# Kernel optimization log

Measured on AMD Instinct MI355X. Metric: run time of the kernel, lower is better.

Reference implementation:

```python
import jax, jax.numpy as jnp
import numpy as np

N_TYPES = 4
N_PAIRS = N_TYPES * N_TYPES          # 16 (src_type, dst_type) pairs
N_GLOBAL_ET = 24                     # global edge event types
N_LOCAL_ET = 16                      # per-pair predictor output classes
D = 256                              # hidden dim
E = 262144                           # number of edges


def setup_inputs() -> dict:
    key = jax.random.key(0)
    ks = jax.random.split(key, 12)
    s = 0.05
    h_src = jax.random.normal(ks[0], (E, D), jnp.float32)
    h_dst = jax.random.normal(ks[1], (E, D), jnp.float32)
    src_type_idx = jax.random.randint(ks[2], (E,), 0, N_TYPES)
    dst_type_idx = jax.random.randint(ks[3], (E,), 0, N_TYPES)
    edge_type_classes = jax.random.randint(ks[4], (E,), 0, N_GLOBAL_ET)
    # decoder params: Linear(concat(h_src,h_dst)) -> D, split into two matrices
    W1 = jax.random.normal(ks[5], (D, D), jnp.float32) * s
    W2 = jax.random.normal(ks[6], (D, D), jnp.float32) * s
    b_dec = jnp.zeros((D,), jnp.float32)
    # per-(src,dst)-pair predictor heads, stacked
    W_pred = jax.random.normal(ks[7], (N_PAIRS, D, N_LOCAL_ET), jnp.float32) * s
    b_pred = jnp.zeros((N_PAIRS, N_LOCAL_ET), jnp.float32)
    # event_map[pair, global_edge_type] -> local class id
    event_map = jax.random.randint(ks[8], (N_PAIRS, N_GLOBAL_ET), 0, N_LOCAL_ET)
    return {
        'h_src': h_src, 'h_dst': h_dst,
        'W1': W1, 'W2': W2, 'b_dec': b_dec,
        'W_pred': W_pred, 'b_pred': b_pred,
        'src_type_idx': src_type_idx, 'dst_type_idx': dst_type_idx,
        'edge_type_classes': edge_type_classes, 'event_map': event_map,
        'inference': 0,
    }


def reference(h_src, h_dst, W1, W2, b_dec, W_pred, b_pred,
              src_type_idx, dst_type_idx, edge_type_classes, event_map,
              inference):
    # decoder: Linear(concat(h_src, h_dst)) -> D, ReLU
    h = jax.nn.relu(h_src @ W1 + h_dst @ W2 + b_dec)            # [E, D]
    pair = src_type_idx * N_TYPES + dst_type_idx                 # [E]
    # grouped per-pair linear heads: compute all heads, select per-edge head
    logits_all = jnp.einsum('ed,pdc->epc', h, W_pred) + b_pred   # [E, P, C]
    logits = jnp.take_along_axis(
        logits_all, pair[:, None, None], axis=1)[:, 0]           # [E, C]
    labels = event_map[pair, edge_type_classes]                  # [E]
    logp = jax.nn.log_softmax(logits, axis=-1)
    per_edge_loss = -jnp.take_along_axis(logp, labels[:, None], axis=1)[:, 0]
    # training path: per-group mean, then mean over non-empty groups
    sums = jax.ops.segment_sum(per_edge_loss, pair, num_segments=N_PAIRS)
    cnts = jax.ops.segment_sum(jnp.ones_like(per_edge_loss), pair,
                               num_segments=N_PAIRS)
    present = cnts > 0
    gmean = jnp.where(present, sums / jnp.maximum(cnts, 1.0), 0.0)
    loss = jnp.sum(gmean) / jnp.sum(present.astype(jnp.float32))
    return loss
```

## Files before the change

kernel.cpp:

```cpp
#include <hip/hip_runtime.h>
#include <stdint.h>

#define E_EDGES 262144
#define TILE_M 128
#define MAX_TILES 2064

typedef unsigned short ushort_t;
typedef __attribute__((ext_vector_type(8))) short short8;
typedef __attribute__((ext_vector_type(4))) float f32x4;

#define OFF_WT   0
#define OFF_WP   (512*256*2)
#define OFF_PERM (OFF_WP + 16*8*64*8*2)
#define OFF_HIST (OFF_PERM + MAX_TILES*128*4)
#define OFF_SEG  (OFF_HIST + 64)
#define OFF_CUR  (OFF_SEG + 128)
#define OFF_SUMS (OFF_CUR + 64)

__device__ __forceinline__ ushort_t f2bf(float f) {
  union { float f; unsigned u; } c; c.f = f;
  unsigned r = c.u + 0x7fffu + ((c.u >> 16) & 1u);
  return (ushort_t)(r >> 16);
}

__device__ __forceinline__ void async_copy16(void* lds, const void* g) {
  __builtin_amdgcn_global_load_lds(
      (const __attribute__((address_space(1))) unsigned int*)g,
      (__attribute__((address_space(3))) unsigned int*)lds, 16, 0, 0);
}

__global__ __launch_bounds__(256) void prep_k(const float* __restrict__ W1,
    const float* __restrict__ W2, const float* __restrict__ Wp,
    char* __restrict__ ws) {
  const int i = blockIdx.x * 256 + threadIdx.x;
  int* perm = (int*)(ws + OFF_PERM);
  if (i < MAX_TILES * 128) perm[i] = -1;
  if (i < 512 * 256) {
    ushort_t* Wt = (ushort_t*)(ws + OFF_WT);
    const int n = i >> 9, k = i & 511;
    const float v = (k < 256) ? W1[(k << 8) + n] : W2[((k - 256) << 8) + n];
    Wt[i] = f2bf(v);
  }
  if (i < 16 * 8 * 64 * 8) {
    ushort_t* Wpf = (ushort_t*)(ws + OFF_WP);
    const int j = i & 7, l = (i >> 3) & 63, s = (i >> 9) & 7, p = i >> 12;
    const int k = s * 32 + (l >> 4) * 8 + j, c = l & 15;
    Wpf[i] = f2bf(Wp[((p << 8) + k) * 16 + c]);
  }
  if (i < 16) {
    ((int*)(ws + OFF_HIST))[i] = 0;
    ((int*)(ws + OFF_CUR))[i] = 0;
    ((float*)(ws + OFF_SUMS))[i] = 0.f;
  }
}

__global__ __launch_bounds__(256) void hist_k(const int* __restrict__ st,
    const int* __restrict__ dt, char* __restrict__ ws) {
  __shared__ int lh[16];
  int* hist = (int*)(ws + OFF_HIST);
  const int t = threadIdx.x;
  if (t < 16) lh[t] = 0;
  __syncthreads();
  const int i = blockIdx.x * 256 + t;
  if (i < E_EDGES) atomicAdd(&lh[st[i] * 4 + dt[i]], 1);
  __syncthreads();
  if (t < 16 && lh[t] > 0) atomicAdd(&hist[t], lh[t]);
}

__global__ void scan_k(char* __restrict__ ws) {
  if (threadIdx.x == 0) {
    const int* hist = (const int*)(ws + OFF_HIST);
    int* seg = (int*)(ws + OFF_SEG);
    int acc = 0;
    for (int p = 0; p < 16; ++p) {
      seg[p] = acc;
      acc += (hist[p] + 127) & ~127;
    }
    seg[16] = acc;
  }
}

__global__ __launch_bounds__(256) void scatter_k(const int* __restrict__ st,
    const int* __restrict__ dt, char* __restrict__ ws) {
  __shared__ int lh[16], lbase[16];
  const int* seg = (const int*)(ws + OFF_SEG);
  int* cur = (int*)(ws + OFF_CUR);
  int* perm = (int*)(ws + OFF_PERM);
  const int t = threadIdx.x;
  if (t < 16) lh[t] = 0;
  __syncthreads();
  const int i = blockIdx.x * 256 + t;
  int p = 0, r = 0;
  const bool v = (i < E_EDGES);
  if (v) { p = st[i] * 4 + dt[i]; r = atomicAdd(&lh[p], 1); }
  __syncthreads();
  if (t < 16 && lh[t] > 0) lbase[t] = atomicAdd(&cur[t], lh[t]);
  __syncthreads();
  if (v) perm[seg[p] + lbase[p] + r] = i;
}

__global__ __launch_bounds__(512, 4) void main_k(
    const float* __restrict__ h_src, const float* __restrict__ h_dst,
    const float* __restrict__ b_dec, const float* __restrict__ b_pred,
    const int* __restrict__ etc_arr, const int* __restrict__ emap,
    char* __restrict__ ws) {
  const ushort_t* Wt = (const ushort_t*)(ws + OFF_WT);
  const short8* Wpf = (const short8*)(ws + OFF_WP);
  const int* perm = (const int*)(ws + OFF_PERM);
  const int* seg = (const int*)(ws + OFF_SEG);
  float* sums = (float*)(ws + OFF_SUMS);

  const int tb = blockIdx.x * TILE_M;
  if (tb >= seg[16]) return;
  int pair = 0;
#pragma unroll
  for (int p = 1; p < 16; ++p) pair += (tb >= seg[p]) ? 1 : 0;

  __shared__ __align__(16) char smem[65536];
  ushort_t* A_buf0 = (ushort_t*)smem;
  ushort_t* A_buf1 = (ushort_t*)(smem + 10240);
  char* B_buf0 = smem + 20480;
  char* B_buf1 = smem + 36864;
  ushort_t* H_ls = (ushort_t*)smem;

  const int t = threadIdx.x;
  const int w = t >> 6, lane = t & 63;
  const int quad = lane >> 4, l15 = lane & 15;
  const int wm = w >> 2, wn = w & 3;

  const int arow = t >> 2, acg = t & 3;
  const int e_stage = perm[tb + arow];
  const int e_safe = (e_stage < 0) ? 0 : e_stage;

  const f32x4 zero4 = {0.f, 0.f, 0.f, 0.f};
  f32x4 acc[4][4];
#pragma unroll
  for (int i = 0; i < 4; ++i)
#pragma unroll
    for (int j = 0; j < 4; ++j) acc[i][j] = zero4;

  auto stage_B = [&](int kt, char* Bb) {
#pragma unroll
    for (int ci = 0; ci < 2; ++ci) {
      const int chunk = w * 2 + ci;
      const int n = chunk * 16 + l15;
      const int k = kt * 32 + quad * 8;
      async_copy16(Bb + chunk * 1024, Wt + n * 512 + k);
    }
  };
  auto gather_A = [&](int kt, f32x4* fv) {
    const float* srcb = (kt < 8) ? h_src : h_dst;
    const f32x4* gp = (const f32x4*)(srcb + ((size_t)e_safe << 8) + (kt & 7) * 32 + acg * 8);
    fv[0] = gp[0];
    fv[1] = gp[1];
  };
  auto conv_write = [&](const f32x4* fv, ushort_t* Ab) {
    union { ushort_t u[8]; short8 v; } pk;
#pragma unroll
    for (int q = 0; q < 2; ++q)
#pragma unroll
      for (int x = 0; x < 4; ++x) pk.u[q * 4 + x] = f2bf(fv[q][x]);
    *(short8*)(Ab + arow * 40 + acg * 8) = pk.v;
  };
  auto mma_step = [&](const ushort_t* Ab, const char* Bb) {
    short8 a[4];
#pragma unroll
    for (int i = 0; i < 4; ++i)
      a[i] = *(const short8*)(Ab + (wm * 64 + i * 16 + l15) * 40 + quad * 8);
#pragma unroll
    for (int j = 0; j < 4; ++j) {
      const short8 b = *(const short8*)(Bb + (wn * 4 + j) * 1024 + lane * 16);
#pragma unroll
      for (int i = 0; i < 4; ++i)
        acc[i][j] = __builtin_amdgcn_mfma_f32_16x16x32_bf16(a[i], b, acc[i][j], 0, 0, 0);
    }
  };

  f32x4 ga0[2], ga1[2];
  gather_A(0, ga0);
  __builtin_amdgcn_sched_barrier(0);
  stage_B(0, B_buf0);
  __builtin_amdgcn_sched_barrier(0);
  gather_A(1, ga1);
  __builtin_amdgcn_sched_barrier(0);
  conv_write(ga0, A_buf0);
  asm volatile("s_waitcnt vmcnt(2) lgkmcnt(0)" ::: "memory");
  __builtin_amdgcn_s_barrier();
  __builtin_amdgcn_sched_barrier(0);

#pragma unroll
  for (int kt = 0; kt < 15; ++kt) {
    ushort_t* Acur = (kt & 1) ? A_buf1 : A_buf0;
    ushort_t* Anxt = (kt & 1) ? A_buf0 : A_buf1;
    char* Bcur = (kt & 1) ? B_buf1 : B_buf0;
    char* Bnxt = (kt & 1) ? B_buf0 : B_buf1;
    f32x4* g_nxt = (kt & 1) ? ga0 : ga1;
    f32x4* g_new = (kt & 1) ? ga1 : ga0;

    stage_B(kt + 1, Bnxt);
    __builtin_amdgcn_sched_barrier(0);
    gather_A(kt + 2, g_new);
    __builtin_amdgcn_sched_barrier(0);
    mma_step(Acur, Bcur);
    asm volatile("s_waitcnt vmcnt(4)" ::: "memory");
    conv_write(g_nxt, Anxt);
    asm volatile("s_waitcnt vmcnt(2) lgkmcnt(0)" ::: "memory");
    __builtin_amdgcn_s_barrier();
    __builtin_amdgcn_sched_barrier(0);
  }
  mma_step(A_buf1, B_buf1);
  __syncthreads();

  float bj[4];
#pragma unroll
  for (int j = 0; j < 4; ++j) bj[j] = b_dec[wn * 64 + j * 16 + l15];
#pragma unroll
  for (int i = 0; i < 4; ++i)
#pragma unroll
    for (int j = 0; j < 4; ++j)
#pragma unroll
      for (int r = 0; r < 4; ++r) {
        const int row = wm * 64 + i * 16 + quad * 4 + r;
        const int col = wn * 64 + j * 16 + l15;
        float v = acc[i][j][r] + bj[j];
        v = fmaxf(v, 0.f);
        H_ls[row * 256 + col] = f2bf(v);
      }
  __syncthreads();

  f32x4 acc2 = zero4;
#pragma unroll
  for (int s = 0; s < 8; ++s) {
    short8 a = *(const short8*)(H_ls + (w * 16 + l15) * 256 + s * 32 + quad * 8);
    short8 b = Wpf[(pair * 8 + s) * 64 + lane];
    acc2 = __builtin_amdgcn_mfma_f32_16x16x32_bf16(a, b, acc2, 0, 0, 0);
  }

  const float bp = b_pred[pair * 16 + l15];
  float wacc = 0.f;
#pragma unroll
  for (int r = 0; r < 4; ++r) {
    const int row = w * 16 + quad * 4 + r;
    const int e = perm[tb + row];
    float v = acc2[r] + bp;
    float m = v;
#pragma unroll
    for (int o = 1; o < 16; o <<= 1) m = fmaxf(m, __shfl_xor(m, o, 16));
    float sm = __expf(v - m);
#pragma unroll
    for (int o = 1; o < 16; o <<= 1) sm += __shfl_xor(sm, o, 16);
    int label = 0;
    if (e >= 0) label = emap[pair * 24 + etc_arr[e]];
    const float vlab = __shfl(v, (lane & 48) + label, 64);
    if (e >= 0 && l15 == 0) wacc += m + __logf(sm) - vlab;
  }
  wacc += __shfl_xor(wacc, 16, 64);
  wacc += __shfl_xor(wacc, 32, 64);
  if (lane == 0) atomicAdd(&sums[pair], wacc);
}

__global__ void finalize_k(const char* __restrict__ ws, float* __restrict__ out) {
  const float* sums = (const float*)(ws + OFF_SUMS);
  const int* hist = (const int*)(ws + OFF_HIST);
  const int t = threadIdx.x;
  float g = 0.f, pr = 0.f;
  if (t < 16) {
    const int c = hist[t];
    if (c > 0) { g = sums[t] / (float)c; pr = 1.f; }
  }
#pragma unroll
  for (int o = 1; o < 16; o <<= 1) { g += __shfl_xor(g, o, 64); pr += __shfl_xor(pr, o, 64); }
  if (t == 0) out[0] = g / pr;
}

extern "C" void kernel_launch(void* const* d_in, const int* in_sizes, int n_in,
                              void* d_out, int out_size, void* d_ws, size_t ws_size,
                              hipStream_t stream) {
  const float* h_src  = (const float*)d_in[0];
  const float* h_dst  = (const float*)d_in[1];
  const float* W1     = (const float*)d_in[2];
  const float* W2     = (const float*)d_in[3];
  const float* b_dec  = (const float*)d_in[4];
  const float* W_pred = (const float*)d_in[5];
  const float* b_pred = (const float*)d_in[6];
  const int* st   = (const int*)d_in[7];
  const int* dt   = (const int*)d_in[8];
  const int* etc  = (const int*)d_in[9];
  const int* emap = (const int*)d_in[10];
  char* ws = (char*)d_ws;
  float* out = (float*)d_out;

  prep_k<<<(MAX_TILES * 128 + 255) / 256, 256, 0, stream>>>(W1, W2, W_pred, ws);
  hist_k<<<E_EDGES / 256, 256, 0, stream>>>(st, dt, ws);
  scan_k<<<1, 64, 0, stream>>>(ws);
  scatter_k<<<E_EDGES / 256, 256, 0, stream>>>(st, dt, ws);
  main_k<<<MAX_TILES, 512, 0, stream>>>(h_src, h_dst, b_dec, b_pred, etc, emap, ws);
  finalize_k<<<1, 64, 0, stream>>>(ws, out);
}
```

Before: 740.8 us.

## Compute all pair heads per tile and drop the edge sorting pipeline

Removes the histogram, scan and scatter kernels that grouped edges by pair, and processes edges in their natural order. Each tile now computes logits for all 16 pair heads with a 128x256 MFMA GEMM and selects each edge's head per row, accumulating per-pair sums and counts in shared memory before global atomics. It also adds an XOR swizzle to the H tile in LDS to reduce bank conflicts. This trades extra MFMA work on the second GEMM for removing three kernel launches, the permutation indirection, padding tiles and scattered gathers.

Measured after the change: 612.3 us. 1.21x faster.

```diff
diff --git a/kernel.cpp b/kernel.cpp
--- a/kernel.cpp
+++ b/kernel.cpp
@@ -3,7 +3,7 @@
 
 #define E_EDGES 262144
 #define TILE_M 128
-#define MAX_TILES 2064
+#define NBLK (E_EDGES / TILE_M)
 
 typedef unsigned short ushort_t;
 typedef __attribute__((ext_vector_type(8))) short short8;
@@ -11,11 +11,8 @@
 
 #define OFF_WT   0
 #define OFF_WP   (512*256*2)
-#define OFF_PERM (OFF_WP + 16*8*64*8*2)
-#define OFF_HIST (OFF_PERM + MAX_TILES*128*4)
-#define OFF_SEG  (OFF_HIST + 64)
-#define OFF_CUR  (OFF_SEG + 128)
-#define OFF_SUMS (OFF_CUR + 64)
+#define OFF_HIST (OFF_WP + 8*16*64*8*2)
+#define OFF_SUMS (OFF_HIST + 64)
 
 __device__ __forceinline__ ushort_t f2bf(float f) {
   union { float f; unsigned u; } c; c.f = f;
@@ -33,90 +30,40 @@
     const float* __restrict__ W2, const float* __restrict__ Wp,
     char* __restrict__ ws) {
   const int i = blockIdx.x * 256 + threadIdx.x;
-  int* perm = (int*)(ws + OFF_PERM);
-  if (i < MAX_TILES * 128) perm[i] = -1;
   if (i < 512 * 256) {
     ushort_t* Wt = (ushort_t*)(ws + OFF_WT);
     const int n = i >> 9, k = i & 511;
     const float v = (k < 256) ? W1[(k << 8) + n] : W2[((k - 256) << 8) + n];
     Wt[i] = f2bf(v);
   }
-  if (i < 16 * 8 * 64 * 8) {
+  if (i < 8 * 16 * 64 * 8) {
     ushort_t* Wpf = (ushort_t*)(ws + OFF_WP);
-    const int j = i & 7, l = (i >> 3) & 63, s = (i >> 9) & 7, p = i >> 12;
-    const int k = s * 32 + (l >> 4) * 8 + j, c = l & 15;
+    const int jj = i & 7, l = (i >> 3) & 63, p = (i >> 9) & 15, s = i >> 13;
+    const int k = s * 32 + (l >> 4) * 8 + jj, c = l & 15;
     Wpf[i] = f2bf(Wp[((p << 8) + k) * 16 + c]);
   }
   if (i < 16) {
     ((int*)(ws + OFF_HIST))[i] = 0;
-    ((int*)(ws + OFF_CUR))[i] = 0;
     ((float*)(ws + OFF_SUMS))[i] = 0.f;
   }
-}
-
-__global__ __launch_bounds__(256) void hist_k(const int* __restrict__ st,
-    const int* __restrict__ dt, char* __restrict__ ws) {
-  __shared__ int lh[16];
-  int* hist = (int*)(ws + OFF_HIST);
-  const int t = threadIdx.x;
-  if (t < 16) lh[t] = 0;
-  __syncthreads();
-  const int i = blockIdx.x * 256 + t;
-  if (i < E_EDGES) atomicAdd(&lh[st[i] * 4 + dt[i]], 1);
-  __syncthreads();
-  if (t < 16 && lh[t] > 0) atomicAdd(&hist[t], lh[t]);
-}
-
-__global__ void scan_k(char* __restrict__ ws) {
-  if (threadIdx.x == 0) {
-    const int* hist = (const int*)(ws + OFF_HIST);
-    int* seg = (int*)(ws + OFF_SEG);
-    int acc = 0;
-    for (int p = 0; p < 16; ++p) {
-      seg[p] = acc;
-      acc += (hist[p] + 127) & ~127;
-    }
-    seg[16] = acc;
-  }
-}
-
-__global__ __launch_bounds__(256) void scatter_k(const int* __restrict__ st,
-    const int* __restrict__ dt, char* __restrict__ ws) {
-  __shared__ int lh[16], lbase[16];
-  const int* seg = (const int*)(ws + OFF_SEG);
-  int* cur = (int*)(ws + OFF_CUR);
-  int* perm = (int*)(ws + OFF_PERM);
-  const int t = threadIdx.x;
-  if (t < 16) lh[t] = 0;
-  __syncthreads();
-  const int i = blockIdx.x * 256 + t;
-  int p = 0, r = 0;
-  const bool v = (i < E_EDGES);
-  if (v) { p = st[i] * 4 + dt[i]; r = atomicAdd(&lh[p], 1); }
-  __syncthreads();
-  if (t < 16 && lh[t] > 0) lbase[t] = atomicAdd(&cur[t], lh[t]);
-  __syncthreads();
-  if (v) perm[seg[p] + lbase[p] + r] = i;
 }
 
 __global__ __launch_bounds__(512, 4) void main_k(
     const float* __restrict__ h_src, const float* __restrict__ h_dst,
     const float* __restrict__ b_dec, const float* __restrict__ b_pred,
+    const int* __restrict__ st, const int* __restrict__ dt,
     const int* __restrict__ etc_arr, const int* __restrict__ emap,
     char* __restrict__ ws) {
   const ushort_t* Wt = (const ushort_t*)(ws + OFF_WT);
-  const short8* Wpf = (const short8*)(ws + OFF_WP);
-  const int* perm = (const int*)(ws + OFF_PERM);
-  const int* seg = (const int*)(ws + OFF_SEG);
+  const short8* Wpf2 = (const short8*)(ws + OFF_WP);
+  int* hist = (int*)(ws + OFF_HIST);
   float* sums = (float*)(ws + OFF_SUMS);
 
   const int tb = blockIdx.x * TILE_M;
-  if (tb >= seg[16]) return;
-  int pair = 0;
-#pragma unroll
-  for (int p = 1; p < 16; ++p) pair += (tb >= seg[p]) ? 1 : 0;
 
   __shared__ __align__(16) char smem[65536];
+  __shared__ float lsums[16];
+  __shared__ int lcnts[16];
   ushort_t* A_buf0 = (ushort_t*)smem;
   ushort_t* A_buf1 = (ushort_t*)(smem + 10240);
   char* B_buf0 = smem + 20480;
@@ -129,8 +76,9 @@
   const int wm = w >> 2, wn = w & 3;
 
   const int arow = t >> 2, acg = t & 3;
-  const int e_stage = perm[tb + arow];
-  const int e_safe = (e_stage < 0) ? 0 : e_stage;
+  const int e_row = tb + arow;
+
+  if (t < 16) { lsums[t] = 0.f; lcnts[t] = 0; }
 
   const f32x4 zero4 = {0.f, 0.f, 0.f, 0.f};
   f32x4 acc[4][4];
@@ -150,7 +98,7 @@
   };
   auto gather_A = [&](int kt, f32x4* fv) {
     const float* srcb = (kt < 8) ? h_src : h_dst;
-    const f32x4* gp = (const f32x4*)(srcb + ((size_t)e_safe << 8) + (kt & 7) * 32 + acg * 8);
+    const f32x4* gp = (const f32x4*)(srcb + ((size_t)e_row << 8) + (kt & 7) * 32 + acg * 8);
     fv[0] = gp[0];
     fv[1] = gp[1];
   };
@@ -224,39 +172,83 @@
         const int col = wn * 64 + j * 16 + l15;
         float v = acc[i][j][r] + bj[j];
         v = fmaxf(v, 0.f);
-        H_ls[row * 256 + col] = f2bf(v);
+        H_ls[row * 256 + (((col >> 3) ^ (row & 7)) << 3) + (col & 7)] = f2bf(v);
       }
   __syncthreads();
 
-  f32x4 acc2 = zero4;
+  f32x4 acc2[4][4];
+#pragma unroll
+  for (int i = 0; i < 4; ++i)
+#pragma unroll
+    for (int j = 0; j < 4; ++j) acc2[i][j] = zero4;
 #pragma unroll
   for (int s = 0; s < 8; ++s) {
-    short8 a = *(const short8*)(H_ls + (w * 16 + l15) * 256 + s * 32 + quad * 8);
-    short8 b = Wpf[(pair * 8 + s) * 64 + lane];
-    acc2 = __builtin_amdgcn_mfma_f32_16x16x32_bf16(a, b, acc2, 0, 0, 0);
-  }
-
-  const float bp = b_pred[pair * 16 + l15];
-  float wacc = 0.f;
-#pragma unroll
-  for (int r = 0; r < 4; ++r) {
-    const int row = w * 16 + quad * 4 + r;
-    const int e = perm[tb + row];
-    float v = acc2[r] + bp;
-    float m = v;
-#pragma unroll
-    for (int o = 1; o < 16; o <<= 1) m = fmaxf(m, __shfl_xor(m, o, 16));
-    float sm = __expf(v - m);
-#pragma unroll
-    for (int o = 1; o < 16; o <<= 1) sm += __shfl_xor(sm, o, 16);
-    int label = 0;
-    if (e >= 0) label = emap[pair * 24 + etc_arr[e]];
-    const float vlab = __shfl(v, (lane & 48) + label, 64);
-    if (e >= 0 && l15 == 0) wacc += m + __logf(sm) - vlab;
-  }
-  wacc += __shfl_xor(wacc, 16, 64);
-  wacc += __shfl_xor(wacc, 32, 64);
-  if (lane == 0) atomicAdd(&sums[pair], wacc);
+    short8 a[4], b[4];
+#pragma unroll
+    for (int x = 0; x < 4; ++x) {
+      const int row = wm * 64 + x * 16 + l15;
+      a[x] = *(const short8*)(H_ls + row * 256 + (((s * 4 + quad) ^ (row & 7)) << 3));
+    }
+#pragma unroll
+    for (int j = 0; j < 4; ++j)
+      b[j] = Wpf2[(s * 16 + wn * 4 + j) * 64 + lane];
+#pragma unroll
+    for (int x = 0; x < 4; ++x)
+#pragma unroll
+      for (int j = 0; j < 4; ++j)
+        acc2[x][j] = __builtin_amdgcn_mfma_f32_16x16x32_bf16(a[x], b[j], acc2[x][j], 0, 0, 0);
+  }
+
+  float bpj[4];
+#pragma unroll
+  for (int j = 0; j < 4; ++j) bpj[j] = b_pred[(wn * 4 + j) * 16 + l15];
+  float wsum[4] = {0.f, 0.f, 0.f, 0.f};
+  int wcnt[4] = {0, 0, 0, 0};
+#pragma unroll
+  for (int i = 0; i < 4; ++i)
+#pragma unroll
+    for (int r = 0; r < 4; ++r) {
+      const int row = wm * 64 + i * 16 + quad * 4 + r;
+      const int e = tb + row;
+      const int pe = st[e] * 4 + dt[e];
+      float v = 0.f;
+#pragma unroll
+      for (int j = 0; j < 4; ++j) {
+        const bool hit = (pe == wn * 4 + j);
+        v = hit ? (acc2[i][j][r] + bpj[j]) : v;
+      }
+      float m = v;
+#pragma unroll
+      for (int o = 1; o < 16; o <<= 1) m = fmaxf(m, __shfl_xor(m, o, 16));
+      float sm = __expf(v - m);
+#pragma unroll
+      for (int o = 1; o < 16; o <<= 1) sm += __shfl_xor(sm, o, 16);
+      const int label = emap[pe * 24 + etc_arr[e]];
+      const float vlab = __shfl(v, (lane & 48) + label, 64);
+      const float loss = m + __logf(sm) - vlab;
+#pragma unroll
+      for (int j = 0; j < 4; ++j)
+        if (pe == wn * 4 + j && l15 == 0) { wsum[j] += loss; wcnt[j] += 1; }
+    }
+  __syncthreads();
+#pragma unroll
+  for (int j = 0; j < 4; ++j) {
+    float wv = wsum[j];
+    int cv = wcnt[j];
+    wv += __shfl_xor(wv, 16, 64);
+    wv += __shfl_xor(wv, 32, 64);
+    cv += __shfl_xor(cv, 16, 64);
+    cv += __shfl_xor(cv, 32, 64);
+    if (lane == 0 && cv > 0) {
+      atomicAdd(&lsums[wn * 4 + j], wv);
+      atomicAdd(&lcnts[wn * 4 + j], cv);
+    }
+  }
+  __syncthreads();
+  if (t < 16 && lcnts[t] > 0) {
+    atomicAdd(&sums[t], lsums[t]);
+    atomicAdd(&hist[t], lcnts[t]);
+  }
 }
 
 __global__ void finalize_k(const char* __restrict__ ws, float* __restrict__ out) {
@@ -290,10 +282,7 @@
   char* ws = (char*)d_ws;
   float* out = (float*)d_out;
 
-  prep_k<<<(MAX_TILES * 128 + 255) / 256, 256, 0, stream>>>(W1, W2, W_pred, ws);
-  hist_k<<<E_EDGES / 256, 256, 0, stream>>>(st, dt, ws);
-  scan_k<<<1, 64, 0, stream>>>(ws);
-  scatter_k<<<E_EDGES / 256, 256, 0, stream>>>(st, dt, ws);
-  main_k<<<MAX_TILES, 512, 0, stream>>>(h_src, h_dst, b_dec, b_pred, etc, emap, ws);
+  prep_k<<<512, 256, 0, stream>>>(W1, W2, W_pred, ws);
+  main_k<<<NBLK, 512, 0, stream>>>(h_src, h_dst, b_dec, b_pred, st, dt, etc, emap, ws);
   finalize_k<<<1, 64, 0, stream>>>(ws, out);
 }
```
